# Kernel tuning notes

Hardware: AMD Instinct MI355X
Metric: run time of the kernel (lower is better)

The kernel has to match this reference:

```python
import jax, jax.numpy as jnp
import numpy as np

# physical / init constants (from DPINeuron.__init__ with default 1e-12 currents)
I0 = 5e-13
UT = 0.025
KAPPA = (0.75 + 0.66) / 2  # 0.705
CMEM, CAMPA, CSHUNT = 3e-12, 2e-12, 2e-12
ITAU_MEM = 1e-12
IGAIN_MEM = 1e-12
ITAU_AMPA = 1e-12
IGAIN_AMPA = 1e-12
ITH = 1e-12
IPFB_TH = 1e-12
IPFB_NORM = 1e-12
REFP = 0.0
DT = 0.001
TAU_MEM = UT / KAPPA * CMEM / ITAU_MEM
TAU_AMPA = UT / KAPPA * CAMPA / ITAU_AMPA
TAU_SHUNT = UT / KAPPA * CSHUNT / ITAU_AMPA
SLOPE = 25.0  # fast_sigmoid surrogate slope

@jax.custom_vjp
def ste_round(x):
    return jnp.round(x)

def _round_fwd(x):
    return jnp.round(x), None

def _round_bwd(_, g):
    return (g,)  # straight-through estimator

ste_round.defvjp(_round_fwd, _round_bwd)

@jax.custom_vjp
def fast_sigmoid(x):
    return (x > 0).astype(x.dtype)

def _fs_fwd(x):
    return (x > 0).astype(x.dtype), x

def _fs_bwd(x, g):
    return (g / (SLOPE * jnp.abs(x) + 1.0) ** 2,)

fast_sigmoid.defvjp(_fs_fwd, _fs_bwd)

B, N_IN, N_OUT = 4096, 2048, 2048

def setup_inputs() -> dict:
    key = jax.random.key(0)
    k1, = jax.random.split(key, 1)
    X = (jax.random.uniform(k1, (B, N_IN), dtype=jnp.float32) < 0.1).astype(jnp.float32)  # sparse input spikes
    return {
        "X": X,
        "W_ampa": jnp.ones((N_OUT, N_IN), jnp.float32),   # init.constant_(1.0)
        "W_shunt": jnp.ones((N_OUT, N_IN), jnp.float32),
        "Imem": jnp.full((B, N_OUT), I0, jnp.float32),    # initialize(): zeros + I0
        "Iampa": jnp.full((B, N_OUT), I0, jnp.float32),
        "Ishunt": jnp.full((B, N_OUT), I0, jnp.float32),
        "refractory": jnp.zeros((B, N_OUT), jnp.float32),
        "Idc": jnp.float32(1e-12),
        "Iw_ampa": jnp.float32(1e-12),
        "Iw_shunt": jnp.float32(1e-12),
        "alpha": jnp.float32(IGAIN_MEM / ITAU_MEM),       # 1.0
        "beta": jnp.float32(1.0 + I0 / ITAU_MEM),         # 1.5
    }

def reference(X, W_ampa, W_shunt, Imem, Iampa, Ishunt, refractory,
              Idc, Iw_ampa, Iw_shunt, alpha, beta):
    Iahp = I0
    Inmda = I0
    # synapse projections with STE-rounded weights: [B, n_out]
    numSynAmpa = jnp.einsum('bi,oi->bo', X, ste_round(W_ampa))
    numSynShunt = jnp.einsum('bi,oi->bo', X, ste_round(W_shunt))

    dIampa = -Iampa / TAU_AMPA
    Iampa = Iampa + (IGAIN_AMPA / ITAU_AMPA) * Iw_ampa * numSynAmpa
    dIshunt = -Ishunt / TAU_SHUNT
    Ishunt = Ishunt + (IGAIN_AMPA / ITAU_AMPA) * Iw_shunt * numSynShunt

    Iin = Idc + Iampa + Inmda - Ishunt
    Iin = Iin * (refractory <= 0)
    Iin = jnp.maximum(Iin, I0)

    Ifb = (I0 ** (1.0 / (KAPPA + 1.0))) * Imem ** (KAPPA / (KAPPA + 1.0)) \
          / (1.0 + jnp.exp(-IPFB_NORM * (Imem - IPFB_TH)))
    f_imem = Ifb / ITAU_MEM * (Imem + IGAIN_MEM)
    dImem = (alpha * (Iin - ITAU_MEM - Iahp) - beta * Imem
             + jax.lax.stop_gradient(f_imem)) / (TAU_MEM * (1.0 + IGAIN_MEM / Imem))
    Imem = jnp.maximum(Imem + dImem * DT, I0)

    # note: original code applies dIshunt decay to Iampa (kept faithful)
    Iampa = jnp.maximum(Iampa + dIampa * DT, I0)
    Iampa = jnp.maximum(Iampa + dIshunt * DT, I0)

    spike = fast_sigmoid(Imem - ITH)
    Imem = (1.0 - spike) * Imem + spike * I0
    refractory = jnp.maximum(refractory - DT, 0.0)
    refractory = (1.0 - spike) * refractory + spike * REFP
    return spike, Imem, Iampa, Ishunt, refractory
```

## Files before the change

### kernel.cpp

```cpp
#include <hip/hip_runtime.h>
#include <cmath>

#ifndef __has_builtin
#define __has_builtin(x) 0
#endif

#define B_DIM 4096
#define K_DIM 2048
#define N_DIM 2048

#define BM 128
#define BN 128
#define BK 64

typedef __attribute__((ext_vector_type(4))) float f32x4;
typedef __attribute__((ext_vector_type(4))) int i32x4;
typedef __attribute__((ext_vector_type(16))) signed char i8x16;


__device__ __forceinline__ signed char f2i8(float f) {
    int t = __float2int_rn(f);
    t = t < -127 ? -127 : (t > 127 ? 127 : t);
    return (signed char)t;
}

__device__ __forceinline__ void gl2lds16(const void* g, void* l) {
#if __has_builtin(__builtin_amdgcn_global_load_lds)
    __builtin_amdgcn_global_load_lds((__attribute__((address_space(1))) void*)g,
                                     (__attribute__((address_space(3))) void*)l,
                                     16, 0, 0);
#else
    *(uint4*)l = *(const uint4*)g;
#endif
}

#define VMWAIT_(n) asm volatile("s_waitcnt vmcnt(" #n ")" ::: "memory")
#define VMWAIT(n)  VMWAIT_(n)
#define FENCE      asm volatile("" ::: "memory")
#define SBARRIER   do { FENCE; __builtin_amdgcn_s_barrier(); FENCE; } while (0)


__global__ void cast_all_kernel(const float* __restrict__ X,
                                const float* __restrict__ Wa,
                                const float* __restrict__ Ws,
                                signed char* __restrict__ Xb,
                                signed char* __restrict__ Wab,
                                signed char* __restrict__ Wsb) {
    const int bid = blockIdx.x;
    if (bid < 2048) {
        size_t i = ((size_t)bid * 256 + threadIdx.x) * 16;
        i8x16 o;
#pragma unroll
        for (int j = 0; j < 16; j += 4) {
            f32x4 a = *(const f32x4*)(X + i + j);
            o[j]     = f2i8(a[0]);
            o[j + 1] = f2i8(a[1]);
            o[j + 2] = f2i8(a[2]);
            o[j + 3] = f2i8(a[3]);
        }
        *(i8x16*)(Xb + i) = o;
    } else {
        size_t i = ((size_t)(bid - 2048) * 256 + threadIdx.x) * 16;
        i8x16 oa, os;
#pragma unroll
        for (int j = 0; j < 16; j += 4) {
            f32x4 a = *(const f32x4*)(Wa + i + j);
            f32x4 s = *(const f32x4*)(Ws + i + j);
            oa[j]     = f2i8(a[0]); oa[j + 1] = f2i8(a[1]);
            oa[j + 2] = f2i8(a[2]); oa[j + 3] = f2i8(a[3]);
            os[j]     = f2i8(s[0]); os[j + 1] = f2i8(s[1]);
            os[j + 2] = f2i8(s[2]); os[j + 3] = f2i8(s[3]);
        }
        *(i8x16*)(Wab + i) = oa;
        *(i8x16*)(Wsb + i) = os;
    }
}


#define RS 132

__device__ __forceinline__ void stage_tile(int tt, int bufIdx, int tid, int m0, int n0,
                                           unsigned char* smem,
                                           const signed char* __restrict__ Xb,
                                           const signed char* __restrict__ Wab,
                                           const signed char* __restrict__ Wsb) {
    unsigned char* bb = smem + bufIdx * 24576;
    const int k0s = tt * BK;
#pragma unroll
    for (int j = 0; j < 2; j++) {
        const int c   = j * 256 + tid;
        const int row = c >> 2;
        const int js  = (c & 3) ^ ((row >> 1) & 3);
        gl2lds16(Xb + (size_t)(m0 + row) * K_DIM + k0s + js * 16, bb + c * 16);
    }
#pragma unroll
    for (int j = 0; j < 2; j++) {
        const int c   = j * 256 + tid;
        const int row = c >> 2;
        const int js  = (c & 3) ^ ((row >> 1) & 3);
        const size_t go = (size_t)(n0 + row) * K_DIM + k0s + js * 16;
        gl2lds16(Wab + go, bb + 8192  + c * 16);
        gl2lds16(Wsb + go, bb + 16384 + c * 16);
    }
}

#define TILE_STEP(t_, rb_, sb_, WAITN, DOSTG)                                 \
{                                                                             \
  VMWAIT(WAITN); SBARRIER;                                                    \
  const unsigned char* bb = smem + (rb_) * 24576;                             \
  const signed char* sA  = (const signed char*)bb;                            \
  const signed char* sWa = (const signed char*)(bb + 8192);                   \
  const signed char* sWs = (const signed char*)(bb + 16384);                  \
  i32x4 af[4], ba[4], bs[4];                                                  \
  _Pragma("unroll") for (int mi = 0; mi < 4; mi++)                            \
      af[mi] = *(const i32x4*)(sA + (wm + mi * 16 + frow) * 64 + slot16);     \
  _Pragma("unroll") for (int ni = 0; ni < 4; ni++) {                          \
      const int o = (wn + ni * 16 + frow) * 64 + slot16;                      \
      ba[ni] = *(const i32x4*)(sWa + o);                                      \
      bs[ni] = *(const i32x4*)(sWs + o);                                      \
  }                                                                           \
  if (DOSTG) stage_tile((t_) + 2, (sb_), tid, m0, n0, smem, Xb, Wab, Wsb);    \
  __builtin_amdgcn_sched_barrier(0);                                          \
  _Pragma("unroll") for (int mi = 0; mi < 4; mi++)                            \
  _Pragma("unroll") for (int ni = 0; ni < 4; ni++) {                          \
      accA[mi][ni] = __builtin_amdgcn_mfma_i32_16x16x64_i8(af[mi], ba[ni], accA[mi][ni], 0, 0, 0); \
      accS[mi][ni] = __builtin_amdgcn_mfma_i32_16x16x64_i8(af[mi], bs[ni], accS[mi][ni], 0, 0, 0); \
  }                                                                           \
}

__global__ __launch_bounds__(256, 2)
void dpi_fused_kernel(const signed char* __restrict__ Xb,
                      const signed char* __restrict__ Wab,
                      const signed char* __restrict__ Wsb,
                      const float* __restrict__ gImem,
                      const float* __restrict__ gIampa,
                      const float* __restrict__ gIshunt,
                      const float* __restrict__ gRefr,
                      const float* __restrict__ pIdc,
                      const float* __restrict__ pIwa,
                      const float* __restrict__ pIws,
                      const float* __restrict__ pAlpha,
                      const float* __restrict__ pBeta,
                      float* __restrict__ out,
                      float i0pow, float kexp, float tau_mem, float inv_tau_syn)
{
    __shared__ __align__(16) unsigned char smem[73728];
    float* na_buf = (float*)smem;
    float* ns_buf = (float*)(smem + 16896);

    const int tid  = threadIdx.x;
    const int lane = tid & 63;
    const int wave = tid >> 6;

    const int lin = blockIdx.x;
    const int xcd = lin & 7;
    const int loc = lin >> 3;
    const int mb  = (xcd & 3) * 8 + (loc & 7);
    const int nb  = (xcd >> 2) * 8 + (loc >> 3);
    const int m0  = mb * BM;
    const int n0  = nb * BN;

    const int wm = (wave & 1) * 64;
    const int wn = (wave >> 1) * 64;

    i32x4 accA[4][4], accS[4][4];
#pragma unroll
    for (int i = 0; i < 4; i++)
#pragma unroll
        for (int j = 0; j < 4; j++) { accA[i][j] = (i32x4)0; accS[i][j] = (i32x4)0; }

    const int frow   = lane & 15;
    const int kq     = lane >> 4;
    const int slot16 = (kq ^ ((frow >> 1) & 3)) * 16;

    stage_tile(0, 0, tid, m0, n0, smem, Xb, Wab, Wsb); FENCE;
    stage_tile(1, 1, tid, m0, n0, smem, Xb, Wab, Wsb); FENCE;

    for (int tb = 0; tb < 30; tb += 3) {
        TILE_STEP(tb + 0, 0, 2, 6, 1);
        TILE_STEP(tb + 1, 1, 0, 6, 1);
        TILE_STEP(tb + 2, 2, 1, 6, 1);
    }
    TILE_STEP(30, 0, 2, 6, 0);
    TILE_STEP(31, 1, 0, 0, 0);

    SBARRIER;

    const float idc   = *pIdc;
    const float iwa   = *pIwa;
    const float iws   = *pIws;
    const float alpha = *pAlpha;
    const float beta  = *pBeta;

    const size_t plane = (size_t)B_DIM * N_DIM;
    float* __restrict__ oSpike = out;
    float* __restrict__ oImem  = out + plane;
    float* __restrict__ oIampa = out + 2 * plane;
    float* __restrict__ oIsh   = out + 3 * plane;
    float* __restrict__ oRefr  = out + 4 * plane;

    const int rowgroup = wm >> 6;
    const int quad4    = (lane >> 4) << 2;
    const int cseg     = (tid & 31) * 4;
    const int rgrp     = tid >> 5;

#pragma unroll
    for (int s = 0; s < 4; s++) {
#pragma unroll
        for (int ni = 0; ni < 4; ni++) {
            const int lcol = wn + ni * 16 + (lane & 15);
#pragma unroll
            for (int r = 0; r < 4; r++) {
                const int lrow = rowgroup * 16 + quad4 + r;
                na_buf[lrow * RS + lcol] = (float)accA[s][ni][r];
                ns_buf[lrow * RS + lcol] = (float)accS[s][ni][r];
            }
        }
        __syncthreads();

#pragma unroll
        for (int q = 0; q < 4; q++) {
            const int lrow = rgrp * 4 + q;
            const int grow = m0 + (lrow >> 4) * 64 + s * 16 + (lrow & 15);
            const size_t idx = (size_t)grow * N_DIM + n0 + cseg;

            const f32x4 na4 = *(const f32x4*)(na_buf + lrow * RS + cseg);
            const f32x4 ns4 = *(const f32x4*)(ns_buf + lrow * RS + cseg);
            const f32x4 im4 = *(const f32x4*)(gImem   + idx);
            const f32x4 ia4 = *(const f32x4*)(gIampa  + idx);
            const f32x4 is4 = *(const f32x4*)(gIshunt + idx);
            const f32x4 rf4 = *(const f32x4*)(gRefr   + idx);

            f32x4 sp_o, im_o, ia_o, is_o, rf_o;
#pragma unroll
            for (int e = 0; e < 4; e++) {
                const float na  = na4[e];
                const float ns  = ns4[e];
                const float im  = im4[e];
                const float ia  = ia4[e];
                const float ish = is4[e];
                const float rf  = rf4[e];

                const float dIampa  = -ia * inv_tau_syn;
                const float ia2     = ia + iwa * na;
                const float dIshunt = -ish * inv_tau_syn;
                const float ish2    = ish + iws * ns;

                float Iin = idc + ia2 + 5e-13f - ish2;
                Iin = (rf <= 0.0f) ? Iin : 0.0f;
                Iin = fmaxf(Iin, 5e-13f);

                const float ifb = i0pow *
                    __builtin_amdgcn_exp2f(kexp * __builtin_amdgcn_logf(im)) * 0.5f;
                const float fimem = ifb * 1e12f * (im + 1e-12f);
                const float dImem = (alpha * ((Iin - 1e-12f) - 5e-13f) - beta * im + fimem)
                                    / (tau_mem * (1.0f + 1e-12f / im));
                float im2 = fmaxf(im + dImem * 0.001f, 5e-13f);

                float ia3 = fmaxf(ia2 + dIampa * 0.001f, 5e-13f);
                ia3       = fmaxf(ia3 + dIshunt * 0.001f, 5e-13f);

                const float spike = (im2 - 1e-12f > 0.0f) ? 1.0f : 0.0f;
                im2 = (spike > 0.0f) ? 5e-13f : im2;
                float rf2 = fmaxf(rf - 0.001f, 0.0f);
                rf2 = (spike > 0.0f) ? 0.0f : rf2;

                sp_o[e] = spike; im_o[e] = im2; ia_o[e] = ia3;
                is_o[e] = ish2;  rf_o[e] = rf2;
            }

            *(f32x4*)(oSpike + idx) = sp_o;
            *(f32x4*)(oImem  + idx) = im_o;
            *(f32x4*)(oIampa + idx) = ia_o;
            *(f32x4*)(oIsh   + idx) = is_o;
            *(f32x4*)(oRefr  + idx) = rf_o;
        }
        __syncthreads();
    }
}


extern "C" void kernel_launch(void* const* d_in, const int* in_sizes, int n_in,
                              void* d_out, int out_size, void* d_ws, size_t ws_size,
                              hipStream_t stream) {
    (void)in_sizes; (void)n_in; (void)out_size; (void)ws_size;

    const float* X       = (const float*)d_in[0];
    const float* W_ampa  = (const float*)d_in[1];
    const float* W_shunt = (const float*)d_in[2];
    const float* Imem    = (const float*)d_in[3];
    const float* Iampa   = (const float*)d_in[4];
    const float* Ishunt  = (const float*)d_in[5];
    const float* Refr    = (const float*)d_in[6];
    const float* pIdc    = (const float*)d_in[7];
    const float* pIwa    = (const float*)d_in[8];
    const float* pIws    = (const float*)d_in[9];
    const float* pAlpha  = (const float*)d_in[10];
    const float* pBeta   = (const float*)d_in[11];

    signed char* Xb  = (signed char*)d_ws;
    signed char* Wab = Xb  + (size_t)B_DIM * K_DIM;
    signed char* Wsb = Wab + (size_t)N_DIM * K_DIM;

    const float i0pow       = (float)std::pow(5e-13, 1.0 / 1.705);
    const float kexp        = (float)(0.705 / 1.705);
    const float tau_mem     = (float)(0.025 / 0.705 * 3.0);
    const float inv_tau_syn = (float)(1.0 / (0.025 / 0.705 * 2.0));

    cast_all_kernel<<<dim3(3072), dim3(256), 0, stream>>>(
        X, W_ampa, W_shunt, Xb, Wab, Wsb);

    dpi_fused_kernel<<<dim3(512), dim3(256), 0, stream>>>(
        Xb, Wab, Wsb, Imem, Iampa, Ishunt, Refr,
        pIdc, pIwa, pIws, pAlpha, pBeta,
        (float*)d_out, i0pow, kexp, tau_mem, inv_tau_syn);
}
```

Before: 365.7 us.

## Double M tile to 256 with 512-thread blocks to share weight tiles

Doubles the block tile along the batch dimension (BM 128 to 256) and runs 8 waves per block instead of 4, halving the grid to 256 blocks. Each weight tile loaded into LDS now feeds twice as many rows of X, which cuts global and L2 traffic for the two weight matrices. Staging, LDS buffer sizes, the XCD block mapping and the epilogue row mapping are rewritten to match. In exchange the kernel uses more LDS per block, and with only 256 blocks it may not fill all CUs or keep two blocks resident per CU.

New measurement: 353.0 us. 1.04x faster.

```diff
diff --git a/kernel.cpp b/kernel.cpp
--- a/kernel.cpp
+++ b/kernel.cpp
@@ -9,7 +9,7 @@
 #define K_DIM 2048
 #define N_DIM 2048
 
-#define BM 128
+#define BM 256
 #define BN 128
 #define BK 64
 
@@ -78,39 +78,38 @@
 
 
 #define RS 132
+#define BUFSZ 32768
 
 __device__ __forceinline__ void stage_tile(int tt, int bufIdx, int tid, int m0, int n0,
                                            unsigned char* smem,
                                            const signed char* __restrict__ Xb,
                                            const signed char* __restrict__ Wab,
                                            const signed char* __restrict__ Wsb) {
-    unsigned char* bb = smem + bufIdx * 24576;
+    unsigned char* bb = smem + bufIdx * BUFSZ;
     const int k0s = tt * BK;
 #pragma unroll
     for (int j = 0; j < 2; j++) {
-        const int c   = j * 256 + tid;
+        const int c   = j * 512 + tid;
         const int row = c >> 2;
         const int js  = (c & 3) ^ ((row >> 1) & 3);
         gl2lds16(Xb + (size_t)(m0 + row) * K_DIM + k0s + js * 16, bb + c * 16);
     }
-#pragma unroll
-    for (int j = 0; j < 2; j++) {
-        const int c   = j * 256 + tid;
-        const int row = c >> 2;
-        const int js  = (c & 3) ^ ((row >> 1) & 3);
+    {
+        const int row = tid >> 2;
+        const int js  = (tid & 3) ^ ((row >> 1) & 3);
         const size_t go = (size_t)(n0 + row) * K_DIM + k0s + js * 16;
-        gl2lds16(Wab + go, bb + 8192  + c * 16);
-        gl2lds16(Wsb + go, bb + 16384 + c * 16);
+        gl2lds16(Wab + go, bb + 16384 + tid * 16);
+        gl2lds16(Wsb + go, bb + 24576 + tid * 16);
     }
 }
 
 #define TILE_STEP(t_, rb_, sb_, WAITN, DOSTG)                                 \
 {                                                                             \
   VMWAIT(WAITN); SBARRIER;                                                    \
-  const unsigned char* bb = smem + (rb_) * 24576;                             \
+  const unsigned char* bb = smem + (rb_) * BUFSZ;                             \
   const signed char* sA  = (const signed char*)bb;                            \
-  const signed char* sWa = (const signed char*)(bb + 8192);                   \
-  const signed char* sWs = (const signed char*)(bb + 16384);                  \
+  const signed char* sWa = (const signed char*)(bb + 16384);                  \
+  const signed char* sWs = (const signed char*)(bb + 24576);                  \
   i32x4 af[4], ba[4], bs[4];                                                  \
   _Pragma("unroll") for (int mi = 0; mi < 4; mi++)                            \
       af[mi] = *(const i32x4*)(sA + (wm + mi * 16 + frow) * 64 + slot16);     \
@@ -128,7 +127,7 @@
   }                                                                           \
 }
 
-__global__ __launch_bounds__(256, 2)
+__global__ __launch_bounds__(512, 2)
 void dpi_fused_kernel(const signed char* __restrict__ Xb,
                       const signed char* __restrict__ Wab,
                       const signed char* __restrict__ Wsb,
@@ -144,9 +143,9 @@
                       float* __restrict__ out,
                       float i0pow, float kexp, float tau_mem, float inv_tau_syn)
 {
-    __shared__ __align__(16) unsigned char smem[73728];
+    __shared__ __align__(16) unsigned char smem[98304];
     float* na_buf = (float*)smem;
-    float* ns_buf = (float*)(smem + 16896);
+    float* ns_buf = (float*)(smem + 33792);
 
     const int tid  = threadIdx.x;
     const int lane = tid & 63;
@@ -155,13 +154,13 @@
     const int lin = blockIdx.x;
     const int xcd = lin & 7;
     const int loc = lin >> 3;
-    const int mb  = (xcd & 3) * 8 + (loc & 7);
-    const int nb  = (xcd >> 2) * 8 + (loc >> 3);
+    const int mb  = (xcd & 1) * 8 + (loc >> 2);
+    const int nb  = (xcd >> 1) * 4 + (loc & 3);
     const int m0  = mb * BM;
     const int n0  = nb * BN;
 
-    const int wm = (wave & 1) * 64;
-    const int wn = (wave >> 1) * 64;
+    const int wm = (wave >> 1) * 64;
+    const int wn = (wave & 1) * 64;
 
     i32x4 accA[4][4], accS[4][4];
 #pragma unroll
@@ -177,11 +176,11 @@
     stage_tile(1, 1, tid, m0, n0, smem, Xb, Wab, Wsb); FENCE;
 
     for (int tb = 0; tb < 30; tb += 3) {
-        TILE_STEP(tb + 0, 0, 2, 6, 1);
-        TILE_STEP(tb + 1, 1, 0, 6, 1);
-        TILE_STEP(tb + 2, 2, 1, 6, 1);
-    }
-    TILE_STEP(30, 0, 2, 6, 0);
+        TILE_STEP(tb + 0, 0, 2, 4, 1);
+        TILE_STEP(tb + 1, 1, 0, 4, 1);
+        TILE_STEP(tb + 2, 2, 1, 4, 1);
+    }
+    TILE_STEP(30, 0, 2, 4, 0);
     TILE_STEP(31, 1, 0, 0, 0);
 
     SBARRIER;
@@ -199,21 +198,24 @@
     float* __restrict__ oIsh   = out + 3 * plane;
     float* __restrict__ oRefr  = out + 4 * plane;
 
-    const int rowgroup = wm >> 6;
-    const int quad4    = (lane >> 4) << 2;
-    const int cseg     = (tid & 31) * 4;
-    const int rgrp     = tid >> 5;
+    const int quad4 = (lane >> 4) << 2;
+    const int cseg  = (tid & 31) * 4;
+    const int rgrp  = tid >> 5;
 
 #pragma unroll
     for (int s = 0; s < 4; s++) {
-#pragma unroll
-        for (int ni = 0; ni < 4; ni++) {
-            const int lcol = wn + ni * 16 + (lane & 15);
-#pragma unroll
-            for (int r = 0; r < 4; r++) {
-                const int lrow = rowgroup * 16 + quad4 + r;
-                na_buf[lrow * RS + lcol] = (float)accA[s][ni][r];
-                ns_buf[lrow * RS + lcol] = (float)accS[s][ni][r];
+        if ((wave >> 1) == s) {
+#pragma unroll
+            for (int mi = 0; mi < 4; mi++)
+#pragma unroll
+            for (int ni = 0; ni < 4; ni++) {
+                const int lcol = wn + ni * 16 + (lane & 15);
+#pragma unroll
+                for (int r = 0; r < 4; r++) {
+                    const int lrow = mi * 16 + quad4 + r;
+                    na_buf[lrow * RS + lcol] = (float)accA[mi][ni][r];
+                    ns_buf[lrow * RS + lcol] = (float)accS[mi][ni][r];
+                }
             }
         }
         __syncthreads();
@@ -221,7 +223,7 @@
 #pragma unroll
         for (int q = 0; q < 4; q++) {
             const int lrow = rgrp * 4 + q;
-            const int grow = m0 + (lrow >> 4) * 64 + s * 16 + (lrow & 15);
+            const int grow = m0 + s * 64 + lrow;
             const size_t idx = (size_t)grow * N_DIM + n0 + cseg;
 
             const f32x4 na4 = *(const f32x4*)(na_buf + lrow * RS + cseg);
@@ -310,7 +312,7 @@
     cast_all_kernel<<<dim3(3072), dim3(256), 0, stream>>>(
         X, W_ampa, W_shunt, Xb, Wab, Wsb);
 
-    dpi_fused_kernel<<<dim3(512), dim3(256), 0, stream>>>(
+    dpi_fused_kernel<<<dim3(256), dim3(512), 0, stream>>>(
         Xb, Wab, Wsb, Imem, Iampa, Ishunt, Refr,
         pIdc, pIwa, pIws, pAlpha, pBeta,
         (float*)d_out, i0pow, kexp, tau_mem, inv_tau_syn);
```
